# Performance work log

Measured on AMD Instinct MI355X. Metric: run time of the kernel, lower is better.

## Reference

```python
import jax, jax.numpy as jnp
import numpy as np

N = 1_000_000
INC = 128
OUTC = 128
NUM_SEG = 4096
GROUPS = 32
ACN_EPS = 1e-3      # ACN eps
CLAMP_MIN = 1e-3    # .clamp(min=0.001)
GN_EPS = 1e-5       # torch GroupNorm default eps


def setup_inputs() -> dict:
    key = jax.random.key(0)
    ks = jax.random.split(key, 8)
    x = jax.random.normal(ks[0], (N, INC), dtype=jnp.float32)
    weight_pri = jax.random.uniform(ks[1], (N,), dtype=jnp.float32)
    segment_idx = jnp.sort(jax.random.randint(ks[2], (N,), 0, NUM_SEG)).astype(jnp.int64)
    W_conv = (jax.random.normal(ks[3], (INC, OUTC), dtype=jnp.float32) * 0.02)
    b_conv = jnp.zeros((OUTC,), jnp.float32)
    W_att = (jax.random.normal(ks[4], (OUTC, 1), dtype=jnp.float32) * 0.02)
    b_att = jnp.zeros((1,), jnp.float32)
    gamma = jnp.ones((OUTC,), jnp.float32)
    beta = jnp.zeros((OUTC,), jnp.float32)
    return {"x": x, "weight_pri": weight_pri, "W_conv": W_conv, "b_conv": b_conv,
            "W_att": W_att, "b_att": b_att, "gamma": gamma, "beta": beta,
            "segment_idx": segment_idx}


def reference(x, weight_pri, W_conv, b_conv, W_att, b_att, gamma, beta, segment_idx):
    # conv: Linear(inc, outc)
    h = x @ W_conv + b_conv                                  # [N, OUTC]

    # --- ACN ---
    att = h @ W_att + b_att                                  # [N, 1]
    # scatter_softmax over segments (numerically stable)
    seg_max = jax.ops.segment_max(att, segment_idx, num_segments=NUM_SEG)
    e = jnp.exp(att - seg_max[segment_idx])
    a = e / jax.ops.segment_sum(e, segment_idx, num_segments=NUM_SEG)[segment_idx]
    a = a * weight_pri[:, None]
    denom = jnp.maximum(jax.ops.segment_sum(a, segment_idx, num_segments=NUM_SEG), CLAMP_MIN)
    a = a / denom[segment_idx]
    # segment-weighted mean / variance normalization
    mean = jax.ops.segment_sum(h * a, segment_idx, num_segments=NUM_SEG)   # [S, OUTC]
    out = h - mean[segment_idx]
    std = jnp.sqrt(jax.ops.segment_sum(a * out * out, segment_idx, num_segments=NUM_SEG) + ACN_EPS)
    out = out / std[segment_idx]

    # --- GroupNorm(32, OUTC) on [N, C]: normalize per sample, per group ---
    g = out.reshape(-1, GROUPS, OUTC // GROUPS)
    mu = g.mean(axis=-1, keepdims=True)
    var = g.var(axis=-1, keepdims=True)
    gn = ((g - mu) * jax.lax.rsqrt(var + GN_EPS)).reshape(-1, OUTC)
    gn = gn * gamma + beta

    return jax.nn.relu(gn), a
```

## Files before the change

### kernel.cpp

```cpp
#include <hip/hip_runtime.h>
#include <hip/hip_bf16.h>

#define NPTS 1000000
#define NSEG 4096
#define ATTCAP 2048

#define WS_ATT   0ull
#define WS_FLAG  4000000ull
#define WS_NEED  4000064ull

#define KS_ROWS 16
#define LPAD 136

typedef __attribute__((ext_vector_type(8))) short bf16x8;
typedef __attribute__((ext_vector_type(4))) float f32x4;

__device__ __forceinline__ short f2bfs(float f) {
  union { __hip_bfloat16 b; unsigned short s; } u;
  u.b = __float2bfloat16(f);
  return (short)u.s;
}
__device__ __forceinline__ float bf2f(short h) {
  return __uint_as_float(((unsigned)(unsigned short)h) << 16);
}
__device__ __forceinline__ void online_merge(float& m, float& se, float& sw,
                                             float m2, float se2, float sw2) {
  float nm = fmaxf(m, m2);
  float f1 = __expf(m - nm), f2 = __expf(m2 - nm);
  se = se * f1 + se2 * f2;
  sw = sw * f1 + sw2 * f2;
  m = nm;
}

__device__ __forceinline__ int chbase_of(int wave, int lc) {
  return wave * 32 + (lc >> 1) * 4 + (lc & 1) * 2;
}

__device__ __forceinline__ void load_w2(const float* __restrict__ Wc, int chb, int lg,
                                        bf16x8 Bh[2][4], bf16x8 Bl[2][4]) {
#pragma unroll
  for (int ks = 0; ks < 4; ++ks) {
#pragma unroll
    for (int j = 0; j < 8; ++j) {
      int k = ks * 32 + lg * 8 + j;
      float2 w2 = *(const float2*)(Wc + (size_t)k * 128 + chb);
      float e[2] = {w2.x, w2.y};
#pragma unroll
      for (int c = 0; c < 2; ++c) {
        short hi = f2bfs(e[c]);
        Bh[c][ks][j] = hi;
        Bl[c][ks][j] = f2bfs(e[c] - bf2f(hi));
      }
    }
  }
}

__device__ __forceinline__ void cvt4(float4 v, short4& hi, short4& lo) {
  hi.x = f2bfs(v.x); lo.x = f2bfs(v.x - bf2f(hi.x));
  hi.y = f2bfs(v.y); lo.y = f2bfs(v.y - bf2f(hi.y));
  hi.z = f2bfs(v.z); lo.z = f2bfs(v.z - bf2f(hi.z));
  hi.w = f2bfs(v.w); lo.w = f2bfs(v.w - bf2f(hi.w));
}

__device__ __forceinline__ void mfma_lds(const bf16x8* __restrict__ AHv,
                                         const bf16x8* __restrict__ ALv,
                                         int lc, int lg,
                                         const bf16x8 Bh[2][4], const bf16x8 Bl[2][4],
                                         f32x4 Cf[2]) {
  Cf[0] = (f32x4){0.f, 0.f, 0.f, 0.f};
  Cf[1] = (f32x4){0.f, 0.f, 0.f, 0.f};
#pragma unroll
  for (int ks = 0; ks < 4; ++ks) {
    int fi = lc * 17 + ks * 4 + lg;
    bf16x8 ah = AHv[fi];
    bf16x8 al = ALv[fi];
#pragma unroll
    for (int c = 0; c < 2; ++c) {
      Cf[c] = __builtin_amdgcn_mfma_f32_16x16x32_bf16(ah, Bh[c][ks], Cf[c], 0, 0, 0);
      Cf[c] = __builtin_amdgcn_mfma_f32_16x16x32_bf16(ah, Bl[c][ks], Cf[c], 0, 0, 0);
      Cf[c] = __builtin_amdgcn_mfma_f32_16x16x32_bf16(al, Bh[c][ks], Cf[c], 0, 0, 0);
    }
  }
}

__global__ __launch_bounds__(256) void k_att(
    const float* __restrict__ x, const float* __restrict__ Wc,
    const float* __restrict__ Wa, const void* __restrict__ seg,
    float* __restrict__ att, int* __restrict__ flag) {
  __shared__ float us[128];
  __shared__ int sm_any;
  const int t = threadIdx.x;
  if (blockIdx.x == 0) {
    if (t == 0) sm_any = 0;
    __syncthreads();
    const int* seg32 = (const int*)seg;
    int any = 0;
#pragma unroll
    for (int k = 0; k < 8; ++k) any |= seg32[2 * (t * 8 + k) + 1];
    if (any) sm_any = 1;
    __syncthreads();
    if (t == 0) *flag = (sm_any == 0) ? 1 : 0;
  }
  if (t < 128) {
    const float4* wa4 = (const float4*)Wa;
    const float4* wr  = (const float4*)(Wc + t * 128);
    float s = 0.f;
#pragma unroll 8
    for (int c4 = 0; c4 < 32; ++c4) {
      float4 a = wr[c4], b = wa4[c4];
      s += a.x * b.x + a.y * b.y + a.z * b.z + a.w * b.w;
    }
    us[t] = s;
  }
  __syncthreads();
  const int q8 = t & 7;
  float ur[16];
#pragma unroll
  for (int j = 0; j < 16; ++j) ur[j] = us[q8 * 16 + j];
  for (int row = blockIdx.x * 32 + (t >> 3); row < NPTS; row += gridDim.x * 32) {
    const float4* xp = (const float4*)(x + (size_t)row * 128 + q8 * 16);
    float4 a0 = xp[0], b0 = xp[1], c0 = xp[2], d0 = xp[3];
    float s = a0.x*ur[0] + a0.y*ur[1] + a0.z*ur[2] + a0.w*ur[3]
            + b0.x*ur[4] + b0.y*ur[5] + b0.z*ur[6] + b0.w*ur[7]
            + c0.x*ur[8] + c0.y*ur[9] + c0.z*ur[10]+ c0.w*ur[11]
            + d0.x*ur[12]+ d0.y*ur[13]+ d0.z*ur[14]+ d0.w*ur[15];
    s += __shfl_xor(s, 1, 64);
    s += __shfl_xor(s, 2, 64);
    s += __shfl_xor(s, 4, 64);
    if (q8 == 0) att[row] = s;
  }
}

__global__ __launch_bounds__(256, 4) void k_merged(
    const float* __restrict__ x, const float* __restrict__ wp,
    const float* __restrict__ att, const float* __restrict__ Wc,
    const float* __restrict__ bc, const float* __restrict__ gamma,
    const float* __restrict__ beta, const void* __restrict__ seg,
    const int* __restrict__ flag, float* __restrict__ out) {

  __shared__ float att_l[ATTCAP];
  __shared__ __align__(16) short AH[2][KS_ROWS * LPAD];
  __shared__ __align__(16) short AL[2][KS_ROWS * LPAD];
  __shared__ float sm_red[12];

  const int t = threadIdx.x;
  const int lane = t & 63;
  const int wave = t >> 6;
  const int lc = lane & 15;
  const int lg = lane >> 4;
  const int chb = chbase_of(wave, lc);
  const int s = blockIdx.x;
  const int* seg32 = (const int*)seg;
  const int f64 = *flag;

  int blo = 0, bhi = NPTS;
  while (blo < bhi) {
    int mid = (blo + bhi) >> 1;
    int v = f64 ? (int)((const long long*)seg)[mid] : seg32[mid];
    if (v < s) blo = mid + 1; else bhi = mid;
  }
  const int start = blo;
  bhi = NPTS;
  while (blo < bhi) {
    int mid = (blo + bhi) >> 1;
    int v = f64 ? (int)((const long long*)seg)[mid] : seg32[mid];
    if (v < s + 1) blo = mid + 1; else bhi = mid;
  }
  const int endc = min(blo, start + ATTCAP);
  if (start >= endc) return;
  const int len = endc - start;

  float m = -3.0e38f, se = 0.f, sw = 0.f;
  for (int i = t; i < len; i += 256) {
    float av = att[start + i], w = wp[start + i];
    att_l[i] = av;
    float nm = fmaxf(m, av);
    float sc = __expf(m - nm), e = __expf(av - nm);
    se = se * sc + e;
    sw = sw * sc + e * w;
    m = nm;
  }
#pragma unroll
  for (int o = 1; o < 64; o <<= 1)
    online_merge(m, se, sw, __shfl_xor(m, o, 64), __shfl_xor(se, o, 64), __shfl_xor(sw, o, 64));
  if (lane == 0) { sm_red[wave] = m; sm_red[4 + wave] = se; sm_red[8 + wave] = sw; }
  __syncthreads();
  float gmx = sm_red[0], gse = sm_red[4], gsw = sm_red[8];
#pragma unroll
  for (int i = 1; i < 4; ++i) online_merge(gmx, gse, gsw, sm_red[i], sm_red[4 + i], sm_red[8 + i]);
  const float ratio = gsw / gse;
  const float dn = fmaxf(ratio, 1e-3f);
  const float ka = 1.f / (gse * dn);
  const float Sa = ratio / dn;
  for (int i = t; i < len; i += 256) {
    float a = __expf(att_l[i] - gmx) * wp[start + i] * ka;
    att_l[i] = a;
    out[(size_t)NPTS * 128 + start + i] = a;
  }
  __syncthreads();

  bf16x8 Bh[2][4], Bl[2][4];
  load_w2(Wc, chb, lg, Bh, Bl);
  float2 bias2 = *(const float2*)(bc    + chb);
  float2 gam2  = *(const float2*)(gamma + chb);
  float2 bet2  = *(const float2*)(beta  + chb);
  float bias_r[2] = {bias2.x, bias2.y};

  const int nt = (len + KS_ROWS - 1) / KS_ROWS;

  float macc[2] = {0.f, 0.f}, m2cc[2] = {0.f, 0.f};
  {
    float4 stg[2];
#pragma unroll
    for (int i = 0; i < 2; ++i) {
      int idx = t + i * 256, row = idx >> 5, c4 = idx & 31;
      int rg = start + row; if (rg >= endc) rg = endc - 1;
      stg[i] = *(const float4*)(x + (size_t)rg * 128 + c4 * 4);
    }
#pragma unroll
    for (int i = 0; i < 2; ++i) {
      int idx = t + i * 256, row = idx >> 5, c4 = idx & 31;
      short4 hi, lo;
      cvt4(stg[i], hi, lo);
      *(short4*)&AH[0][row * LPAD + c4 * 4] = hi;
      *(short4*)&AL[0][row * LPAD + c4 * 4] = lo;
    }
    int cur = 0, tl = 0;
    while (1) {
      bool pf = (tl + 1 < nt);
      __syncthreads();
      if (pf) {
        int rbase = start + (tl + 1) * KS_ROWS;
#pragma unroll
        for (int i = 0; i < 2; ++i) {
          int idx = t + i * 256, row = idx >> 5, c4 = idx & 31;
          int rg = rbase + row; if (rg >= endc) rg = endc - 1;
          stg[i] = *(const float4*)(x + (size_t)rg * 128 + c4 * 4);
        }
      }
      {
        f32x4 Cf[2];
        mfma_lds((const bf16x8*)AH[cur], (const bf16x8*)AL[cur], lc, lg, Bh, Bl, Cf);
        int rbase = start + tl * KS_ROWS;
#pragma unroll
        for (int reg = 0; reg < 4; ++reg) {
          int row = rbase + lg * 4 + reg;
          float a = (row < endc) ? att_l[row - start] : 0.f;
#pragma unroll
          for (int c = 0; c < 2; ++c) {
            float h = Cf[c][reg] + bias_r[c];
            macc[c] += a * h;
            m2cc[c] += a * h * h;
          }
        }
      }
      if (!pf) break;
      __syncthreads();
#pragma unroll
      for (int i = 0; i < 2; ++i) {
        int idx = t + i * 256, row = idx >> 5, c4 = idx & 31;
        short4 hi, lo;
        cvt4(stg[i], hi, lo);
        *(short4*)&AH[cur ^ 1][row * LPAD + c4 * 4] = hi;
        *(short4*)&AL[cur ^ 1][row * LPAD + c4 * 4] = lo;
      }
      cur ^= 1; ++tl;
    }
  }

#pragma unroll
  for (int c = 0; c < 2; ++c) {
    macc[c] += __shfl_xor(macc[c], 16, 64);
    macc[c] += __shfl_xor(macc[c], 32, 64);
    m2cc[c] += __shfl_xor(m2cc[c], 16, 64);
    m2cc[c] += __shfl_xor(m2cc[c], 32, 64);
  }
  float mean_r[2], isd_r[2];
#pragma unroll
  for (int c = 0; c < 2; ++c) {
    float var = m2cc[c] - macc[c] * macc[c] * (2.f - Sa);
    mean_r[c] = macc[c];
    isd_r[c] = 1.f / sqrtf(var + 1e-3f);
  }
  __syncthreads();

  {
    float4 stg[2];
#pragma unroll
    for (int i = 0; i < 2; ++i) {
      int idx = t + i * 256, row = idx >> 5, c4 = idx & 31;
      int rg = start + row; if (rg >= endc) rg = endc - 1;
      stg[i] = *(const float4*)(x + (size_t)rg * 128 + c4 * 4);
    }
#pragma unroll
    for (int i = 0; i < 2; ++i) {
      int idx = t + i * 256, row = idx >> 5, c4 = idx & 31;
      short4 hi, lo;
      cvt4(stg[i], hi, lo);
      *(short4*)&AH[0][row * LPAD + c4 * 4] = hi;
      *(short4*)&AL[0][row * LPAD + c4 * 4] = lo;
    }
    int cur = 0, tl = 0;
    while (1) {
      bool pf = (tl + 1 < nt);
      __syncthreads();
      if (pf) {
        int rbase = start + (tl + 1) * KS_ROWS;
#pragma unroll
        for (int i = 0; i < 2; ++i) {
          int idx = t + i * 256, row = idx >> 5, c4 = idx & 31;
          int rg = rbase + row; if (rg >= endc) rg = endc - 1;
          stg[i] = *(const float4*)(x + (size_t)rg * 128 + c4 * 4);
        }
      }
      {
        f32x4 Cf[2];
        mfma_lds((const bf16x8*)AH[cur], (const bf16x8*)AL[cur], lc, lg, Bh, Bl, Cf);
        int rbase = start + tl * KS_ROWS;
#pragma unroll
        for (int reg = 0; reg < 4; ++reg) {
          int row = rbase + lg * 4 + reg;
          float o0 = (Cf[0][reg] + bias_r[0] - mean_r[0]) * isd_r[0];
          float o1 = (Cf[1][reg] + bias_r[1] - mean_r[1]) * isd_r[1];
          float sp = o0 + o1;
          float qp = o0 * o0 + o1 * o1;
          float s4 = sp + __shfl_xor(sp, 1, 64);
          float q4 = qp + __shfl_xor(qp, 1, 64);
          float mu = 0.25f * s4, msq = 0.25f * q4;
          float gsc = 1.f / sqrtf(msq - mu * mu + 1e-5f);
          if (row < endc) {
            float2 v;
            v.x = fmaxf((o0 - mu) * gsc * gam2.x + bet2.x, 0.f);
            v.y = fmaxf((o1 - mu) * gsc * gam2.y + bet2.y, 0.f);
            *(float2*)(out + (size_t)row * 128 + chb) = v;
          }
        }
      }
      if (!pf) break;
      __syncthreads();
#pragma unroll
      for (int i = 0; i < 2; ++i) {
        int idx = t + i * 256, row = idx >> 5, c4 = idx & 31;
        short4 hi, lo;
        cvt4(stg[i], hi, lo);
        *(short4*)&AH[cur ^ 1][row * LPAD + c4 * 4] = hi;
        *(short4*)&AL[cur ^ 1][row * LPAD + c4 * 4] = lo;
      }
      cur ^= 1; ++tl;
    }
  }
}

__device__ __forceinline__ void load_w_split_fb(const float* __restrict__ Wc, int half,
                                                int lc, int lg, bf16x8 Bh[4][4], bf16x8 Bl[4][4]) {
#pragma unroll
  for (int ks = 0; ks < 4; ++ks) {
#pragma unroll
    for (int j = 0; j < 8; ++j) {
      int k = ks * 32 + lg * 8 + j;
      float4 w4 = *(const float4*)(Wc + (size_t)k * 128 + half * 64 + lc * 4);
      float e[4] = {w4.x, w4.y, w4.z, w4.w};
#pragma unroll
      for (int c = 0; c < 4; ++c) {
        short hi = f2bfs(e[c]);
        Bh[c][ks][j] = hi;
        Bl[c][ks][j] = f2bfs(e[c] - bf2f(hi));
      }
    }
  }
}
__device__ __forceinline__ void mfma_h_fb(const float* __restrict__ x, int rbase,
                                          int lc, int lg,
                                          const bf16x8 Bh[4][4], const bf16x8 Bl[4][4],
                                          f32x4 Cf[4]) {
  int rowA = rbase + lc;
  int ra = rowA < NPTS ? rowA : NPTS - 1;
  const float4* xp = (const float4*)(x + (size_t)ra * 128);
  bf16x8 ah[4], al[4];
#pragma unroll
  for (int ks = 0; ks < 4; ++ks) {
    float4 p0 = xp[ks * 8 + lg * 2], p1 = xp[ks * 8 + lg * 2 + 1];
    float e[8] = {p0.x, p0.y, p0.z, p0.w, p1.x, p1.y, p1.z, p1.w};
    bf16x8 vh, vl;
#pragma unroll
    for (int j = 0; j < 8; ++j) {
      short hi = f2bfs(e[j]);
      vh[j] = hi;
      vl[j] = f2bfs(e[j] - bf2f(hi));
    }
    ah[ks] = vh; al[ks] = vl;
  }
#pragma unroll
  for (int c = 0; c < 4; ++c) Cf[c] = (f32x4){0.f,0.f,0.f,0.f};
#pragma unroll
  for (int ks = 0; ks < 4; ++ks)
#pragma unroll
    for (int c = 0; c < 4; ++c) {
      Cf[c] = __builtin_amdgcn_mfma_f32_16x16x32_bf16(ah[ks], Bh[c][ks], Cf[c], 0, 0, 0);
      Cf[c] = __builtin_amdgcn_mfma_f32_16x16x32_bf16(ah[ks], Bl[c][ks], Cf[c], 0, 0, 0);
      Cf[c] = __builtin_amdgcn_mfma_f32_16x16x32_bf16(al[ks], Bh[c][ks], Cf[c], 0, 0, 0);
    }
}
__global__ __launch_bounds__(256, 2) void k_mfma_fb(
    const float* __restrict__ x, const float* __restrict__ wp,
    const float* __restrict__ Wc, const float* __restrict__ bc,
    const float* __restrict__ Wa,
    const float* __restrict__ gamma, const float* __restrict__ beta,
    const void* __restrict__ seg, float* __restrict__ out) {

  __shared__ float att_l[ATTCAP];
  __shared__ float u_l[128];
  __shared__ float red_m[256];
  __shared__ float red_v[256];
  __shared__ float sm_red[12];
  __shared__ int sm_flag;

  const int t = threadIdx.x;
  const int lane = t & 63;
  const int wave = t >> 6;
  const int lc = lane & 15;
  const int lg = lane >> 4;
  const int half = wave & 1;
  const int rsub = wave >> 1;
  const int s = blockIdx.x;
  const int* seg32 = (const int*)seg;

  if (t == 0) sm_flag = 0;
  __syncthreads();
  {
    int any = 0;
#pragma unroll
    for (int k = 0; k < 8; ++k) any |= seg32[2 * (t * 8 + k) + 1];
    if (any) sm_flag = 1;
  }
  __syncthreads();
  const int f64 = (sm_flag == 0);
  __syncthreads();

  int blo = 0, bhi = NPTS;
  while (blo < bhi) {
    int mid = (blo + bhi) >> 1;
    int v = f64 ? (int)((const long long*)seg)[mid] : seg32[mid];
    if (v < s) blo = mid + 1; else bhi = mid;
  }
  const int start = blo;
  bhi = NPTS;
  while (blo < bhi) {
    int mid = (blo + bhi) >> 1;
    int v = f64 ? (int)((const long long*)seg)[mid] : seg32[mid];
    if (v < s + 1) blo = mid + 1; else bhi = mid;
  }
  const int endc = min(blo, start + ATTCAP);
  if (start >= endc) return;
  const int len = endc - start;

  if (t < 128) {
    const float4* wa4 = (const float4*)Wa;
    const float4* wr  = (const float4*)(Wc + t * 128);
    float sv = 0.f;
#pragma unroll 8
    for (int c4 = 0; c4 < 32; ++c4) {
      float4 a = wr[c4], b = wa4[c4];
      sv += a.x * b.x + a.y * b.y + a.z * b.z + a.w * b.w;
    }
    u_l[t] = sv;
  }
  __syncthreads();
  {
    const int q8 = t & 7;
    float ur[16];
#pragma unroll
    for (int j = 0; j < 16; ++j) ur[j] = u_l[q8 * 16 + j];
    for (int r0 = start; r0 < endc; r0 += 32) {
      int row = r0 + (t >> 3);
      int ra = row < NPTS ? row : NPTS - 1;
      const float4* xp = (const float4*)(x + (size_t)ra * 128 + q8 * 16);
      float4 a0 = xp[0], b0 = xp[1], c0 = xp[2], d0 = xp[3];
      float sv = a0.x*ur[0] + a0.y*ur[1] + a0.z*ur[2] + a0.w*ur[3]
               + b0.x*ur[4] + b0.y*ur[5] + b0.z*ur[6] + b0.w*ur[7]
               + c0.x*ur[8] + c0.y*ur[9] + c0.z*ur[10]+ c0.w*ur[11]
               + d0.x*ur[12]+ d0.y*ur[13]+ d0.z*ur[14]+ d0.w*ur[15];
      sv += __shfl_xor(sv, 1, 64);
      sv += __shfl_xor(sv, 2, 64);
      sv += __shfl_xor(sv, 4, 64);
      if (q8 == 0 && row < endc) att_l[row - start] = sv;
    }
  }
  __syncthreads();
  float m = -3.0e38f, se = 0.f, sw = 0.f;
  for (int i = t; i < len; i += 256) {
    float av = att_l[i], w = wp[start + i];
    float nm = fmaxf(m, av);
    float sc = __expf(m - nm), e = __expf(av - nm);
    se = se * sc + e;
    sw = sw * sc + e * w;
    m = nm;
  }
#pragma unroll
  for (int o = 1; o < 64; o <<= 1)
    online_merge(m, se, sw, __shfl_xor(m, o, 64), __shfl_xor(se, o, 64), __shfl_xor(sw, o, 64));
  if (lane == 0) { sm_red[wave] = m; sm_red[4 + wave] = se; sm_red[8 + wave] = sw; }
  __syncthreads();
  float gmx = sm_red[0], gse = sm_red[4], gsw = sm_red[8];
#pragma unroll
  for (int i = 1; i < 4; ++i) online_merge(gmx, gse, gsw, sm_red[i], sm_red[4 + i], sm_red[8 + i]);
  const float ratio = gsw / gse;
  const float dn = fmaxf(ratio, 1e-3f);
  const float ka = 1.f / (gse * dn);
  const float Sa = ratio / dn;
  for (int i = t; i < len; i += 256) {
    float a = __expf(att_l[i] - gmx) * wp[start + i] * ka;
    att_l[i] = a;
    out[(size_t)NPTS * 128 + start + i] = a;
  }
  __syncthreads();

  bf16x8 Bh[4][4], Bl[4][4];
  load_w_split_fb(Wc, half, lc, lg, Bh, Bl);
  float bias_r[4], gam_r[4], bet_r[4];
  *(float4*)bias_r = *(const float4*)(bc    + half * 64 + lc * 4);
  *(float4*)gam_r  = *(const float4*)(gamma + half * 64 + lc * 4);
  *(float4*)bet_r  = *(const float4*)(beta  + half * 64 + lc * 4);

  float macc[4] = {0.f,0.f,0.f,0.f}, m2cc[4] = {0.f,0.f,0.f,0.f};
  for (int r0 = start; r0 < endc; r0 += 32) {
    int rbase = r0 + rsub * 16;
    f32x4 Cf[4];
    mfma_h_fb(x, rbase, lc, lg, Bh, Bl, Cf);
    float a_r[4];
#pragma unroll
    for (int reg = 0; reg < 4; ++reg) {
      int row = rbase + lg * 4 + reg;
      a_r[reg] = (row < endc) ? att_l[row - start] : 0.f;
    }
#pragma unroll
    for (int c = 0; c < 4; ++c)
#pragma unroll
      for (int reg = 0; reg < 4; ++reg) {
        float h = Cf[c][reg] + bias_r[c];
        macc[c] += a_r[reg] * h;
        m2cc[c] += a_r[reg] * h * h;
      }
  }
#pragma unroll
  for (int c = 0; c < 4; ++c) {
    macc[c] += __shfl_xor(macc[c], 16, 64);
    macc[c] += __shfl_xor(macc[c], 32, 64);
    m2cc[c] += __shfl_xor(m2cc[c], 16, 64);
    m2cc[c] += __shfl_xor(m2cc[c], 32, 64);
  }
  if (lane < 16) {
#pragma unroll
    for (int c = 0; c < 4; ++c) {
      red_m[wave * 64 + lc * 4 + c] = macc[c];
      red_v[wave * 64 + lc * 4 + c] = m2cc[c];
    }
  }
  __syncthreads();
  float mean_r[4], isd_r[4];
#pragma unroll
  for (int c = 0; c < 4; ++c) {
    float mn = red_m[wave * 64 + lc * 4 + c] + red_m[(wave ^ 2) * 64 + lc * 4 + c];
    float M2 = red_v[wave * 64 + lc * 4 + c] + red_v[(wave ^ 2) * 64 + lc * 4 + c];
    float var = M2 - mn * mn * (2.f - Sa);
    mean_r[c] = mn;
    isd_r[c] = 1.f / sqrtf(var + 1e-3f);
  }

  for (int r0 = start; r0 < endc; r0 += 32) {
    int rbase = r0 + rsub * 16;
    f32x4 Cf[4];
    mfma_h_fb(x, rbase, lc, lg, Bh, Bl, Cf);
#pragma unroll
    for (int reg = 0; reg < 4; ++reg) {
      int row = rbase + lg * 4 + reg;
      if (row < endc) {
        float o0 = (Cf[0][reg] + bias_r[0] - mean_r[0]) * isd_r[0];
        float o1 = (Cf[1][reg] + bias_r[1] - mean_r[1]) * isd_r[1];
        float o2 = (Cf[2][reg] + bias_r[2] - mean_r[2]) * isd_r[2];
        float o3 = (Cf[3][reg] + bias_r[3] - mean_r[3]) * isd_r[3];
        float mu  = 0.25f * (o0 + o1 + o2 + o3);
        float msq = 0.25f * (o0*o0 + o1*o1 + o2*o2 + o3*o3);
        float gsc = 1.f / sqrtf(msq - mu * mu + 1e-5f);
        float4 v;
        v.x = fmaxf((o0 - mu) * gsc * gam_r[0] + bet_r[0], 0.f);
        v.y = fmaxf((o1 - mu) * gsc * gam_r[1] + bet_r[1], 0.f);
        v.z = fmaxf((o2 - mu) * gsc * gam_r[2] + bet_r[2], 0.f);
        v.w = fmaxf((o3 - mu) * gsc * gam_r[3] + bet_r[3], 0.f);
        *(float4*)(out + (size_t)row * 128 + half * 64 + lc * 4) = v;
      }
    }
  }
}

extern "C" void kernel_launch(void* const* d_in, const int* in_sizes, int n_in,
                              void* d_out, int out_size, void* d_ws, size_t ws_size,
                              hipStream_t stream) {
  const float* x    = (const float*)d_in[0];
  const float* wpri = (const float*)d_in[1];
  const float* Wc   = (const float*)d_in[2];
  const float* bc   = (const float*)d_in[3];
  const float* Wa   = (const float*)d_in[4];
  const float* gm   = (const float*)d_in[6];
  const float* bt   = (const float*)d_in[7];
  const void*  seg  = d_in[8];
  float* out = (float*)d_out;
  (void)in_sizes; (void)n_in; (void)out_size;

  if (ws_size >= WS_NEED) {
    char* ws = (char*)d_ws;
    float* att  = (float*)(ws + WS_ATT);
    int*   flag = (int*)(ws + WS_FLAG);
    k_att<<<2048, 256, 0, stream>>>(x, Wc, Wa, seg, att, flag);
    k_merged<<<NSEG, 256, 0, stream>>>(x, wpri, att, Wc, bc, gm, bt, seg, flag, out);
  } else {
    k_mfma_fb<<<NSEG, 256, 0, stream>>>(x, wpri, Wc, bc, Wa, gm, bt, seg, out);
  }
}
```

Measured before the change: 431.7 us.

## Fuse attention-logit pass into per-segment kernel, drop separate att kernel

Removes the standalone k_att launch and its global att/flag workspace. Each segment block now detects the index width itself, computes u = Wc·Wa, and computes its own attention logits straight into shared memory before the softmax and MFMA passes. This saves one kernel launch and the global write and read of the att array. In exchange, x is read one extra time per block inside the fused kernel, and each block redoes the u and flag computation.

```diff
diff --git a/kernel.cpp b/kernel.cpp
--- a/kernel.cpp
+++ b/kernel.cpp
@@ -4,10 +4,6 @@
 #define NPTS 1000000
 #define NSEG 4096
 #define ATTCAP 2048
-
-#define WS_ATT   0ull
-#define WS_FLAG  4000000ull
-#define WS_NEED  4000064ull
 
 #define KS_ROWS 16
 #define LPAD 136
@@ -83,65 +79,19 @@
   }
 }
 
-__global__ __launch_bounds__(256) void k_att(
-    const float* __restrict__ x, const float* __restrict__ Wc,
-    const float* __restrict__ Wa, const void* __restrict__ seg,
-    float* __restrict__ att, int* __restrict__ flag) {
-  __shared__ float us[128];
-  __shared__ int sm_any;
-  const int t = threadIdx.x;
-  if (blockIdx.x == 0) {
-    if (t == 0) sm_any = 0;
-    __syncthreads();
-    const int* seg32 = (const int*)seg;
-    int any = 0;
-#pragma unroll
-    for (int k = 0; k < 8; ++k) any |= seg32[2 * (t * 8 + k) + 1];
-    if (any) sm_any = 1;
-    __syncthreads();
-    if (t == 0) *flag = (sm_any == 0) ? 1 : 0;
-  }
-  if (t < 128) {
-    const float4* wa4 = (const float4*)Wa;
-    const float4* wr  = (const float4*)(Wc + t * 128);
-    float s = 0.f;
-#pragma unroll 8
-    for (int c4 = 0; c4 < 32; ++c4) {
-      float4 a = wr[c4], b = wa4[c4];
-      s += a.x * b.x + a.y * b.y + a.z * b.z + a.w * b.w;
-    }
-    us[t] = s;
-  }
-  __syncthreads();
-  const int q8 = t & 7;
-  float ur[16];
-#pragma unroll
-  for (int j = 0; j < 16; ++j) ur[j] = us[q8 * 16 + j];
-  for (int row = blockIdx.x * 32 + (t >> 3); row < NPTS; row += gridDim.x * 32) {
-    const float4* xp = (const float4*)(x + (size_t)row * 128 + q8 * 16);
-    float4 a0 = xp[0], b0 = xp[1], c0 = xp[2], d0 = xp[3];
-    float s = a0.x*ur[0] + a0.y*ur[1] + a0.z*ur[2] + a0.w*ur[3]
-            + b0.x*ur[4] + b0.y*ur[5] + b0.z*ur[6] + b0.w*ur[7]
-            + c0.x*ur[8] + c0.y*ur[9] + c0.z*ur[10]+ c0.w*ur[11]
-            + d0.x*ur[12]+ d0.y*ur[13]+ d0.z*ur[14]+ d0.w*ur[15];
-    s += __shfl_xor(s, 1, 64);
-    s += __shfl_xor(s, 2, 64);
-    s += __shfl_xor(s, 4, 64);
-    if (q8 == 0) att[row] = s;
-  }
-}
-
-__global__ __launch_bounds__(256, 4) void k_merged(
+__global__ __launch_bounds__(256, 4) void k_all2(
     const float* __restrict__ x, const float* __restrict__ wp,
-    const float* __restrict__ att, const float* __restrict__ Wc,
-    const float* __restrict__ bc, const float* __restrict__ gamma,
-    const float* __restrict__ beta, const void* __restrict__ seg,
-    const int* __restrict__ flag, float* __restrict__ out) {
+    const float* __restrict__ Wc, const float* __restrict__ bc,
+    const float* __restrict__ Wa,
+    const float* __restrict__ gamma, const float* __restrict__ beta,
+    const void* __restrict__ seg, float* __restrict__ out) {
 
   __shared__ float att_l[ATTCAP];
   __shared__ __align__(16) short AH[2][KS_ROWS * LPAD];
   __shared__ __align__(16) short AL[2][KS_ROWS * LPAD];
+  __shared__ float us[128];
   __shared__ float sm_red[12];
+  __shared__ int sm_flag;
 
   const int t = threadIdx.x;
   const int lane = t & 63;
@@ -151,7 +101,18 @@
   const int chb = chbase_of(wave, lc);
   const int s = blockIdx.x;
   const int* seg32 = (const int*)seg;
-  const int f64 = *flag;
+
+  if (t == 0) sm_flag = 0;
+  __syncthreads();
+  {
+    int any = 0;
+#pragma unroll
+    for (int k = 0; k < 8; ++k) any |= seg32[2 * (t * 8 + k) + 1];
+    if (any) sm_flag = 1;
+  }
+  __syncthreads();
+  const int f64 = (sm_flag == 0);
+  __syncthreads();
 
   int blo = 0, bhi = NPTS;
   while (blo < bhi) {
@@ -170,10 +131,44 @@
   if (start >= endc) return;
   const int len = endc - start;
 
+  if (t < 128) {
+    const float4* wa4 = (const float4*)Wa;
+    const float4* wr  = (const float4*)(Wc + t * 128);
+    float sv = 0.f;
+#pragma unroll 8
+    for (int c4 = 0; c4 < 32; ++c4) {
+      float4 a = wr[c4], b = wa4[c4];
+      sv += a.x * b.x + a.y * b.y + a.z * b.z + a.w * b.w;
+    }
+    us[t] = sv;
+  }
+  __syncthreads();
+
+  {
+    const int q8 = t & 7;
+    float ur[16];
+#pragma unroll
+    for (int j = 0; j < 16; ++j) ur[j] = us[q8 * 16 + j];
+    for (int r0 = start; r0 < endc; r0 += 32) {
+      int row = r0 + (t >> 3);
+      int ra = row < NPTS ? row : NPTS - 1;
+      const float4* xp = (const float4*)(x + (size_t)ra * 128 + q8 * 16);
+      float4 a0 = xp[0], b0 = xp[1], c0 = xp[2], d0 = xp[3];
+      float sv = a0.x*ur[0] + a0.y*ur[1] + a0.z*ur[2] + a0.w*ur[3]
+               + b0.x*ur[4] + b0.y*ur[5] + b0.z*ur[6] + b0.w*ur[7]
+               + c0.x*ur[8] + c0.y*ur[9] + c0.z*ur[10]+ c0.w*ur[11]
+               + d0.x*ur[12]+ d0.y*ur[13]+ d0.z*ur[14]+ d0.w*ur[15];
+      sv += __shfl_xor(sv, 1, 64);
+      sv += __shfl_xor(sv, 2, 64);
+      sv += __shfl_xor(sv, 4, 64);
+      if (q8 == 0 && row < endc) att_l[row - start] = sv;
+    }
+  }
+  __syncthreads();
+
   float m = -3.0e38f, se = 0.f, sw = 0.f;
   for (int i = t; i < len; i += 256) {
-    float av = att[start + i], w = wp[start + i];
-    att_l[i] = av;
+    float av = att_l[i], w = wp[start + i];
     float nm = fmaxf(m, av);
     float sc = __expf(m - nm), e = __expf(av - nm);
     se = se * sc + e;
@@ -351,248 +346,6 @@
   }
 }
 
-__device__ __forceinline__ void load_w_split_fb(const float* __restrict__ Wc, int half,
-                                                int lc, int lg, bf16x8 Bh[4][4], bf16x8 Bl[4][4]) {
-#pragma unroll
-  for (int ks = 0; ks < 4; ++ks) {
-#pragma unroll
-    for (int j = 0; j < 8; ++j) {
-      int k = ks * 32 + lg * 8 + j;
-      float4 w4 = *(const float4*)(Wc + (size_t)k * 128 + half * 64 + lc * 4);
-      float e[4] = {w4.x, w4.y, w4.z, w4.w};
-#pragma unroll
-      for (int c = 0; c < 4; ++c) {
-        short hi = f2bfs(e[c]);
-        Bh[c][ks][j] = hi;
-        Bl[c][ks][j] = f2bfs(e[c] - bf2f(hi));
-      }
-    }
-  }
-}
-__device__ __forceinline__ void mfma_h_fb(const float* __restrict__ x, int rbase,
-                                          int lc, int lg,
-                                          const bf16x8 Bh[4][4], const bf16x8 Bl[4][4],
-                                          f32x4 Cf[4]) {
-  int rowA = rbase + lc;
-  int ra = rowA < NPTS ? rowA : NPTS - 1;
-  const float4* xp = (const float4*)(x + (size_t)ra * 128);
-  bf16x8 ah[4], al[4];
-#pragma unroll
-  for (int ks = 0; ks < 4; ++ks) {
-    float4 p0 = xp[ks * 8 + lg * 2], p1 = xp[ks * 8 + lg * 2 + 1];
-    float e[8] = {p0.x, p0.y, p0.z, p0.w, p1.x, p1.y, p1.z, p1.w};
-    bf16x8 vh, vl;
-#pragma unroll
-    for (int j = 0; j < 8; ++j) {
-      short hi = f2bfs(e[j]);
-      vh[j] = hi;
-      vl[j] = f2bfs(e[j] - bf2f(hi));
-    }
-    ah[ks] = vh; al[ks] = vl;
-  }
-#pragma unroll
-  for (int c = 0; c < 4; ++c) Cf[c] = (f32x4){0.f,0.f,0.f,0.f};
-#pragma unroll
-  for (int ks = 0; ks < 4; ++ks)
-#pragma unroll
-    for (int c = 0; c < 4; ++c) {
-      Cf[c] = __builtin_amdgcn_mfma_f32_16x16x32_bf16(ah[ks], Bh[c][ks], Cf[c], 0, 0, 0);
-      Cf[c] = __builtin_amdgcn_mfma_f32_16x16x32_bf16(ah[ks], Bl[c][ks], Cf[c], 0, 0, 0);
-      Cf[c] = __builtin_amdgcn_mfma_f32_16x16x32_bf16(al[ks], Bh[c][ks], Cf[c], 0, 0, 0);
-    }
-}
-__global__ __launch_bounds__(256, 2) void k_mfma_fb(
-    const float* __restrict__ x, const float* __restrict__ wp,
-    const float* __restrict__ Wc, const float* __restrict__ bc,
-    const float* __restrict__ Wa,
-    const float* __restrict__ gamma, const float* __restrict__ beta,
-    const void* __restrict__ seg, float* __restrict__ out) {
-
-  __shared__ float att_l[ATTCAP];
-  __shared__ float u_l[128];
-  __shared__ float red_m[256];
-  __shared__ float red_v[256];
-  __shared__ float sm_red[12];
-  __shared__ int sm_flag;
-
-  const int t = threadIdx.x;
-  const int lane = t & 63;
-  const int wave = t >> 6;
-  const int lc = lane & 15;
-  const int lg = lane >> 4;
-  const int half = wave & 1;
-  const int rsub = wave >> 1;
-  const int s = blockIdx.x;
-  const int* seg32 = (const int*)seg;
-
-  if (t == 0) sm_flag = 0;
-  __syncthreads();
-  {
-    int any = 0;
-#pragma unroll
-    for (int k = 0; k < 8; ++k) any |= seg32[2 * (t * 8 + k) + 1];
-    if (any) sm_flag = 1;
-  }
-  __syncthreads();
-  const int f64 = (sm_flag == 0);
-  __syncthreads();
-
-  int blo = 0, bhi = NPTS;
-  while (blo < bhi) {
-    int mid = (blo + bhi) >> 1;
-    int v = f64 ? (int)((const long long*)seg)[mid] : seg32[mid];
-    if (v < s) blo = mid + 1; else bhi = mid;
-  }
-  const int start = blo;
-  bhi = NPTS;
-  while (blo < bhi) {
-    int mid = (blo + bhi) >> 1;
-    int v = f64 ? (int)((const long long*)seg)[mid] : seg32[mid];
-    if (v < s + 1) blo = mid + 1; else bhi = mid;
-  }
-  const int endc = min(blo, start + ATTCAP);
-  if (start >= endc) return;
-  const int len = endc - start;
-
-  if (t < 128) {
-    const float4* wa4 = (const float4*)Wa;
-    const float4* wr  = (const float4*)(Wc + t * 128);
-    float sv = 0.f;
-#pragma unroll 8
-    for (int c4 = 0; c4 < 32; ++c4) {
-      float4 a = wr[c4], b = wa4[c4];
-      sv += a.x * b.x + a.y * b.y + a.z * b.z + a.w * b.w;
-    }
-    u_l[t] = sv;
-  }
-  __syncthreads();
-  {
-    const int q8 = t & 7;
-    float ur[16];
-#pragma unroll
-    for (int j = 0; j < 16; ++j) ur[j] = u_l[q8 * 16 + j];
-    for (int r0 = start; r0 < endc; r0 += 32) {
-      int row = r0 + (t >> 3);
-      int ra = row < NPTS ? row : NPTS - 1;
-      const float4* xp = (const float4*)(x + (size_t)ra * 128 + q8 * 16);
-      float4 a0 = xp[0], b0 = xp[1], c0 = xp[2], d0 = xp[3];
-      float sv = a0.x*ur[0] + a0.y*ur[1] + a0.z*ur[2] + a0.w*ur[3]
-               + b0.x*ur[4] + b0.y*ur[5] + b0.z*ur[6] + b0.w*ur[7]
-               + c0.x*ur[8] + c0.y*ur[9] + c0.z*ur[10]+ c0.w*ur[11]
-               + d0.x*ur[12]+ d0.y*ur[13]+ d0.z*ur[14]+ d0.w*ur[15];
-      sv += __shfl_xor(sv, 1, 64);
-      sv += __shfl_xor(sv, 2, 64);
-      sv += __shfl_xor(sv, 4, 64);
-      if (q8 == 0 && row < endc) att_l[row - start] = sv;
-    }
-  }
-  __syncthreads();
-  float m = -3.0e38f, se = 0.f, sw = 0.f;
-  for (int i = t; i < len; i += 256) {
-    float av = att_l[i], w = wp[start + i];
-    float nm = fmaxf(m, av);
-    float sc = __expf(m - nm), e = __expf(av - nm);
-    se = se * sc + e;
-    sw = sw * sc + e * w;
-    m = nm;
-  }
-#pragma unroll
-  for (int o = 1; o < 64; o <<= 1)
-    online_merge(m, se, sw, __shfl_xor(m, o, 64), __shfl_xor(se, o, 64), __shfl_xor(sw, o, 64));
-  if (lane == 0) { sm_red[wave] = m; sm_red[4 + wave] = se; sm_red[8 + wave] = sw; }
-  __syncthreads();
-  float gmx = sm_red[0], gse = sm_red[4], gsw = sm_red[8];
-#pragma unroll
-  for (int i = 1; i < 4; ++i) online_merge(gmx, gse, gsw, sm_red[i], sm_red[4 + i], sm_red[8 + i]);
-  const float ratio = gsw / gse;
-  const float dn = fmaxf(ratio, 1e-3f);
-  const float ka = 1.f / (gse * dn);
-  const float Sa = ratio / dn;
-  for (int i = t; i < len; i += 256) {
-    float a = __expf(att_l[i] - gmx) * wp[start + i] * ka;
-    att_l[i] = a;
-    out[(size_t)NPTS * 128 + start + i] = a;
-  }
-  __syncthreads();
-
-  bf16x8 Bh[4][4], Bl[4][4];
-  load_w_split_fb(Wc, half, lc, lg, Bh, Bl);
-  float bias_r[4], gam_r[4], bet_r[4];
-  *(float4*)bias_r = *(const float4*)(bc    + half * 64 + lc * 4);
-  *(float4*)gam_r  = *(const float4*)(gamma + half * 64 + lc * 4);
-  *(float4*)bet_r  = *(const float4*)(beta  + half * 64 + lc * 4);
-
-  float macc[4] = {0.f,0.f,0.f,0.f}, m2cc[4] = {0.f,0.f,0.f,0.f};
-  for (int r0 = start; r0 < endc; r0 += 32) {
-    int rbase = r0 + rsub * 16;
-    f32x4 Cf[4];
-    mfma_h_fb(x, rbase, lc, lg, Bh, Bl, Cf);
-    float a_r[4];
-#pragma unroll
-    for (int reg = 0; reg < 4; ++reg) {
-      int row = rbase + lg * 4 + reg;
-      a_r[reg] = (row < endc) ? att_l[row - start] : 0.f;
-    }
-#pragma unroll
-    for (int c = 0; c < 4; ++c)
-#pragma unroll
-      for (int reg = 0; reg < 4; ++reg) {
-        float h = Cf[c][reg] + bias_r[c];
-        macc[c] += a_r[reg] * h;
-        m2cc[c] += a_r[reg] * h * h;
-      }
-  }
-#pragma unroll
-  for (int c = 0; c < 4; ++c) {
-    macc[c] += __shfl_xor(macc[c], 16, 64);
-    macc[c] += __shfl_xor(macc[c], 32, 64);
-    m2cc[c] += __shfl_xor(m2cc[c], 16, 64);
-    m2cc[c] += __shfl_xor(m2cc[c], 32, 64);
-  }
-  if (lane < 16) {
-#pragma unroll
-    for (int c = 0; c < 4; ++c) {
-      red_m[wave * 64 + lc * 4 + c] = macc[c];
-      red_v[wave * 64 + lc * 4 + c] = m2cc[c];
-    }
-  }
-  __syncthreads();
-  float mean_r[4], isd_r[4];
-#pragma unroll
-  for (int c = 0; c < 4; ++c) {
-    float mn = red_m[wave * 64 + lc * 4 + c] + red_m[(wave ^ 2) * 64 + lc * 4 + c];
-    float M2 = red_v[wave * 64 + lc * 4 + c] + red_v[(wave ^ 2) * 64 + lc * 4 + c];
-    float var = M2 - mn * mn * (2.f - Sa);
-    mean_r[c] = mn;
-    isd_r[c] = 1.f / sqrtf(var + 1e-3f);
-  }
-
-  for (int r0 = start; r0 < endc; r0 += 32) {
-    int rbase = r0 + rsub * 16;
-    f32x4 Cf[4];
-    mfma_h_fb(x, rbase, lc, lg, Bh, Bl, Cf);
-#pragma unroll
-    for (int reg = 0; reg < 4; ++reg) {
-      int row = rbase + lg * 4 + reg;
-      if (row < endc) {
-        float o0 = (Cf[0][reg] + bias_r[0] - mean_r[0]) * isd_r[0];
-        float o1 = (Cf[1][reg] + bias_r[1] - mean_r[1]) * isd_r[1];
-        float o2 = (Cf[2][reg] + bias_r[2] - mean_r[2]) * isd_r[2];
-        float o3 = (Cf[3][reg] + bias_r[3] - mean_r[3]) * isd_r[3];
-        float mu  = 0.25f * (o0 + o1 + o2 + o3);
-        float msq = 0.25f * (o0*o0 + o1*o1 + o2*o2 + o3*o3);
-        float gsc = 1.f / sqrtf(msq - mu * mu + 1e-5f);
-        float4 v;
-        v.x = fmaxf((o0 - mu) * gsc * gam_r[0] + bet_r[0], 0.f);
-        v.y = fmaxf((o1 - mu) * gsc * gam_r[1] + bet_r[1], 0.f);
-        v.z = fmaxf((o2 - mu) * gsc * gam_r[2] + bet_r[2], 0.f);
-        v.w = fmaxf((o3 - mu) * gsc * gam_r[3] + bet_r[3], 0.f);
-        *(float4*)(out + (size_t)row * 128 + half * 64 + lc * 4) = v;
-      }
-    }
-  }
-}
-
 extern "C" void kernel_launch(void* const* d_in, const int* in_sizes, int n_in,
                               void* d_out, int out_size, void* d_ws, size_t ws_size,
                               hipStream_t stream) {
@@ -605,15 +358,7 @@
   const float* bt   = (const float*)d_in[7];
   const void*  seg  = d_in[8];
   float* out = (float*)d_out;
-  (void)in_sizes; (void)n_in; (void)out_size;
-
-  if (ws_size >= WS_NEED) {
-    char* ws = (char*)d_ws;
-    float* att  = (float*)(ws + WS_ATT);
-    int*   flag = (int*)(ws + WS_FLAG);
-    k_att<<<2048, 256, 0, stream>>>(x, Wc, Wa, seg, att, flag);
-    k_merged<<<NSEG, 256, 0, stream>>>(x, wpri, att, Wc, bc, gm, bt, seg, flag, out);
-  } else {
-    k_mfma_fb<<<NSEG, 256, 0, stream>>>(x, wpri, Wc, bc, Wa, gm, bt, seg, out);
-  }
-}
+  (void)in_sizes; (void)n_in; (void)out_size; (void)d_ws; (void)ws_size;
+
+  k_all2<<<NSEG, 256, 0, stream>>>(x, wpri, Wc, bc, Wa, gm, bt, seg, out);
+}
```

Result: faster. 394.8 us (-8.5%).
